# Optimization experiments

Measured on AMD Instinct MI355X. Metric: run time of the kernel, lower is better.

Reference implementation:

```python
import jax, jax.numpy as jnp
import numpy as np

HIDDEN = 1024
FFN = 2048
NUM_EXPERTS = 8
TOP_K = 2
BATCH, SEQ = 2, 1024


def setup_inputs() -> dict:
    key = jax.random.key(0)
    k0, k1, k2, k3, k4 = jax.random.split(key, 5)
    scale = 0.02
    hidden_states = jax.random.normal(k0, (BATCH, SEQ, HIDDEN), dtype=jnp.float32)
    gate_w = jax.random.normal(k1, (NUM_EXPERTS, HIDDEN), dtype=jnp.float32) * scale
    w1 = jax.random.normal(k2, (NUM_EXPERTS, FFN, HIDDEN), dtype=jnp.float32) * scale  # gate proj
    w3 = jax.random.normal(k3, (NUM_EXPERTS, FFN, HIDDEN), dtype=jnp.float32) * scale  # up proj
    w2 = jax.random.normal(k4, (NUM_EXPERTS, HIDDEN, FFN), dtype=jnp.float32) * scale  # down proj
    return {"hidden_states": hidden_states, "gate_w": gate_w, "w1": w1, "w2": w2, "w3": w3}


def reference(hidden_states, gate_w, w1, w2, w3):
    B, S, D = hidden_states.shape
    x = hidden_states.reshape(-1, D)                         # [T, D]
    T = x.shape[0]
    # Router: logits -> fp32 softmax -> top-k -> renormalize
    router_logits = jnp.einsum("td,ed->te", x, gate_w)       # [T, E]
    routing_weights = jax.nn.softmax(router_logits.astype(jnp.float32), axis=1)
    top_vals, top_idx = jax.lax.top_k(routing_weights, TOP_K)  # [T, K]
    top_vals = top_vals / jnp.sum(top_vals, axis=-1, keepdims=True)
    top_vals = top_vals.astype(x.dtype)
    # Per-token-per-expert combine weight (0 for unselected experts)
    w_te = jnp.zeros((T, NUM_EXPERTS), dtype=x.dtype)
    w_te = w_te.at[jnp.arange(T)[:, None], top_idx].add(top_vals)  # [T, E]
    # Fused experts: silu(x W1^T) * (x W3^T) -> W2^T, weighted combine
    g = jax.nn.silu(jnp.einsum("td,efd->tef", x, w1))        # [T, E, F]
    u = jnp.einsum("td,efd->tef", x, w3)                     # [T, E, F]
    y = jnp.einsum("tef,edf->ted", g * u, w2)                # [T, E, D]
    out = jnp.einsum("ted,te->td", y, w_te)                  # [T, D]
    return out.reshape(B, S, D), router_logits
```

## Files before the change

kernel.cpp:

```cpp
#include <hip/hip_runtime.h>
#include <hip/hip_bf16.h>
#include <stdint.h>

#define HIDDEN  1024
#define FFN_DIM 2048
#define NEXP    8
#define NTOK    2048
#define MAXROWS 5120

typedef short bf16x8 __attribute__((ext_vector_type(8)));
typedef float f32x4  __attribute__((ext_vector_type(4)));

static const size_t OFF_CNT  = 0;
static const size_t OFF_BASE = 64;
static const size_t OFF_TOK  = 128;
static const size_t OFF_WGT  = OFF_TOK + (size_t)NEXP*NTOK*4;
static const size_t OFF_XBF  = 131328;
static const size_t XBF_B    = (size_t)NTOK*HIDDEN*2;
static const size_t OFF_H    = OFF_XBF + XBF_B;
static const size_t H_B      = (size_t)MAXROWS*FFN_DIM*2;
static const size_t WS_NEED  = OFF_H + H_B;

__device__ __forceinline__ unsigned short f2bf(float f) {
  union { float f; unsigned u; } a; a.f = f;
  unsigned r = a.u + 0x7fff + ((a.u >> 16) & 1);
  return (unsigned short)(r >> 16);
}

__device__ __forceinline__ uint4 cvt8(float4 a, float4 b) {
  uint4 r;
  asm("v_cvt_pk_bf16_f32 %0, %1, %2" : "=v"(r.x) : "v"(a.x), "v"(a.y));
  asm("v_cvt_pk_bf16_f32 %0, %1, %2" : "=v"(r.y) : "v"(a.z), "v"(a.w));
  asm("v_cvt_pk_bf16_f32 %0, %1, %2" : "=v"(r.z) : "v"(b.x), "v"(b.y));
  asm("v_cvt_pk_bf16_f32 %0, %1, %2" : "=v"(r.w) : "v"(b.z), "v"(b.w));
  return r;
}

__device__ __forceinline__ void ld_g2l16(const void* gsrc, void* ldst) {
  __builtin_amdgcn_global_load_lds(
      (const __attribute__((address_space(1))) unsigned int*)gsrc,
      (__attribute__((address_space(3))) unsigned int*)ldst, 16, 0, 0);
}

__global__ __launch_bounds__(256) void router_kernel(
    const float* __restrict__ x, const float* __restrict__ gw,
    float* __restrict__ logits, int* __restrict__ cnt,
    int* __restrict__ tok, float* __restrict__ wgt)
{
  const int t   = blockIdx.x;
  const int tid = threadIdx.x;
  float4 xv = ((const float4*)(x + (size_t)t * HIDDEN))[tid];
  float p[NEXP];
#pragma unroll
  for (int e = 0; e < NEXP; ++e) {
    float4 gv = ((const float4*)(gw + (size_t)e * HIDDEN))[tid];
    p[e] = xv.x * gv.x + xv.y * gv.y + xv.z * gv.z + xv.w * gv.w;
  }
#pragma unroll
  for (int e = 0; e < NEXP; ++e) {
#pragma unroll
    for (int off = 32; off > 0; off >>= 1)
      p[e] += __shfl_down(p[e], off, 64);
  }
  __shared__ float red[4][NEXP];
  const int wv = tid >> 6, ln = tid & 63;
  if (ln == 0) {
#pragma unroll
    for (int e = 0; e < NEXP; ++e) red[wv][e] = p[e];
  }
  __syncthreads();
  if (tid == 0) {
    float l[NEXP];
#pragma unroll
    for (int e = 0; e < NEXP; ++e) {
      l[e] = red[0][e] + red[1][e] + red[2][e] + red[3][e];
      logits[(size_t)t * NEXP + e] = l[e];
    }
    int i0 = 0;
#pragma unroll
    for (int e = 1; e < NEXP; ++e) if (l[e] > l[i0]) i0 = e;
    int i1 = (i0 == 0) ? 1 : 0;
#pragma unroll
    for (int e = 0; e < NEXP; ++e) if (e != i0 && l[e] > l[i1]) i1 = e;
    float w0 = 1.f / (1.f + expf(l[i1] - l[i0]));
    float w1 = 1.f - w0;
    int s0 = atomicAdd(&cnt[i0], 1);
    tok[i0 * NTOK + s0] = t;  wgt[i0 * NTOK + s0] = w0;
    int s1 = atomicAdd(&cnt[i1], 1);
    tok[i1 * NTOK + s1] = t;  wgt[i1 * NTOK + s1] = w1;
  }
}

__global__ void prefix_kernel(const int* __restrict__ cnt, int* __restrict__ base) {
  if (threadIdx.x == 0 && blockIdx.x == 0) {
    int b = 0;
#pragma unroll
    for (int e = 0; e < NEXP; ++e) { base[e] = b; b += ((cnt[e] + 63) >> 6) << 6; }
    base[NEXP] = b;
  }
}

__global__ __launch_bounds__(256) void cvt_kernel(
    const float* __restrict__ src, unsigned short* __restrict__ dst, int n4)
{
  int i = blockIdx.x * blockDim.x + threadIdx.x;
  const int stride = gridDim.x * blockDim.x;
  for (; i < n4; i += stride) {
    float4 v = ((const float4*)src)[i];
    ushort4 o;
    o.x = f2bf(v.x); o.y = f2bf(v.y); o.z = f2bf(v.z); o.w = f2bf(v.w);
    ((ushort4*)dst)[i] = o;
  }
}

__global__ __launch_bounds__(512, 4) void gemm1_kernel(
    const unsigned short* __restrict__ xbf,
    const float* __restrict__ w1f,
    const float* __restrict__ w3f,
    const int* __restrict__ cnt, const int* __restrict__ base,
    const int* __restrict__ tok,
    unsigned short* __restrict__ H)
{
  const int bid  = blockIdx.x;
  const int e    = bid & 7;
  const int slot = bid >> 3;
  const int mt   = slot & 31;
  const int nt   = slot >> 5;
  const int n = cnt[e];
  if (mt * 64 >= n) return;
  const int t = threadIdx.x;
  const int w = t >> 6, l = t & 63;

  __shared__ unsigned short Xs [64 * 64];
  __shared__ unsigned short W1s[128 * 64];
  __shared__ unsigned short W3s[128 * 64];

  const int rX = t >> 3;
  const size_t tok0 = (size_t)tok[e * NTOK + min(mt * 64 + rX, n - 1)];
  const int kp = (((t & 7) ^ ((t >> 3) & 7)) << 3);

  const float* w1e = w1f + (size_t)e * FFN_DIM * HIDDEN + (size_t)(nt * 128) * HIDDEN;
  const float* w3e = w3f + (size_t)e * FFN_DIM * HIDDEN + (size_t)(nt * 128) * HIDDEN;
  const float* w1p0 = w1e + (size_t)rX        * HIDDEN + kp;
  const float* w1p1 = w1e + (size_t)(64 + rX) * HIDDEN + kp;
  const float* w3p0 = w3e + (size_t)rX        * HIDDEN + kp;
  const float* w3p1 = w3e + (size_t)(64 + rX) * HIDDEN + kp;

  uint4* lw1a = (uint4*)((char*)W1s + t * 16);
  uint4* lw1b = (uint4*)((char*)W1s + 8192 + t * 16);
  uint4* lw3a = (uint4*)((char*)W3s + t * 16);
  uint4* lw3b = (uint4*)((char*)W3s + 8192 + t * 16);
  char* ldsX = (char*)Xs + w * 1024;

  f32x4 acc1[2][2], acc3[2][2];
#pragma unroll
  for (int i = 0; i < 2; ++i)
#pragma unroll
    for (int j = 0; j < 2; ++j) { acc1[i][j] = (f32x4)0.f; acc3[i][j] = (f32x4)0.f; }

  const int Moff = (w & 1) * 32;
  const int Noff = (w >> 1) * 32;
  const int lr = l & 15;
  const int lg = l >> 4;

  for (int kb = 0; kb < HIDDEN / 64; ++kb) {
    __syncthreads();
    ld_g2l16(xbf + tok0 * HIDDEN + kb * 64 + kp, ldsX);
    {
      const int ko = kb * 64;
      float4 a0 = *(const float4*)(w1p0 + ko);
      float4 a1 = *(const float4*)(w1p0 + ko + 4);
      float4 a2 = *(const float4*)(w1p1 + ko);
      float4 a3 = *(const float4*)(w1p1 + ko + 4);
      float4 b0 = *(const float4*)(w3p0 + ko);
      float4 b1 = *(const float4*)(w3p0 + ko + 4);
      float4 b2 = *(const float4*)(w3p1 + ko);
      float4 b3 = *(const float4*)(w3p1 + ko + 4);
      *lw1a = cvt8(a0, a1);
      *lw1b = cvt8(a2, a3);
      *lw3a = cvt8(b0, b1);
      *lw3b = cvt8(b2, b3);
    }
    __syncthreads();
#pragma unroll
    for (int s = 0; s < 2; ++s) {
      const int ug = 4 * s + lg;
      bf16x8 a[2], b1v[2], b3v[2];
#pragma unroll
      for (int mi = 0; mi < 2; ++mi) {
        const int R = Moff + mi * 16 + lr;
        a[mi] = *(const bf16x8*)&Xs[R * 64 + ((ug ^ (lr & 7)) << 3)];
      }
#pragma unroll
      for (int ni = 0; ni < 2; ++ni) {
        const int R = Noff + ni * 16 + lr;
        b1v[ni] = *(const bf16x8*)&W1s[R * 64 + ((ug ^ (lr & 7)) << 3)];
        b3v[ni] = *(const bf16x8*)&W3s[R * 64 + ((ug ^ (lr & 7)) << 3)];
      }
#pragma unroll
      for (int mi = 0; mi < 2; ++mi)
#pragma unroll
        for (int ni = 0; ni < 2; ++ni) {
          acc1[mi][ni] = __builtin_amdgcn_mfma_f32_16x16x32_bf16(a[mi], b1v[ni], acc1[mi][ni], 0, 0, 0);
          acc3[mi][ni] = __builtin_amdgcn_mfma_f32_16x16x32_bf16(a[mi], b3v[ni], acc3[mi][ni], 0, 0, 0);
        }
    }
  }

  const size_t rbase = (size_t)base[e] + (size_t)mt * 64;
#pragma unroll
  for (int mi = 0; mi < 2; ++mi)
#pragma unroll
    for (int ni = 0; ni < 2; ++ni)
#pragma unroll
      for (int j = 0; j < 4; ++j) {
        int row = Moff + mi * 16 + lg * 4 + j;
        int col = nt * 128 + Noff + ni * 16 + lr;
        float s1 = acc1[mi][ni][j], s3 = acc3[mi][ni][j];
        float h = (s1 / (1.f + __expf(-s1))) * s3;
        H[(rbase + row) * FFN_DIM + col] = f2bf(h);
      }
}

__global__ __launch_bounds__(512, 4) void gemm2_kernel(
    const unsigned short* __restrict__ H,
    const float* __restrict__ w2f,
    const int* __restrict__ cnt, const int* __restrict__ base,
    const int* __restrict__ tok, const float* __restrict__ wgt,
    float* __restrict__ out)
{
  const int bid  = blockIdx.x;
  const int e    = bid & 7;
  const int slot = bid >> 3;
  const int mt   = slot & 31;
  const int nt   = (slot >> 5) & 7;
  const int sk   = slot >> 8;
  const int n = cnt[e];
  if (mt * 64 >= n) return;
  const int t = threadIdx.x;
  const int w = t >> 6, l = t & 63;

  __shared__ unsigned short Hs[64 * 64];
  __shared__ unsigned short Ws[128 * 64];
  __shared__ int   stok[64];
  __shared__ float swgt[64];

  if (t < 64) {
    int idx = mt * 64 + t;
    int ok = idx < n;
    stok[t] = ok ? tok[e * NTOK + idx] : -1;
    swgt[t] = ok ? wgt[e * NTOK + idx] : 0.f;
  }

  const int rH = t >> 3;
  const int kp = (((t & 7) ^ ((t >> 3) & 7)) << 3);
  const unsigned short* He = H + (size_t)(base[e] + mt * 64) * FFN_DIM;
  const float* w2e  = w2f + (size_t)e * HIDDEN * FFN_DIM + (size_t)(nt * 128) * FFN_DIM;
  const float* w2p0 = w2e + (size_t)rH        * FFN_DIM + kp;
  const float* w2p1 = w2e + (size_t)(64 + rH) * FFN_DIM + kp;

  uint4* lwa = (uint4*)((char*)Ws + t * 16);
  uint4* lwb = (uint4*)((char*)Ws + 8192 + t * 16);
  char* ldsH = (char*)Hs + w * 1024;

  f32x4 acc[2][2];
#pragma unroll
  for (int i = 0; i < 2; ++i)
#pragma unroll
    for (int j = 0; j < 2; ++j) acc[i][j] = (f32x4)0.f;

  const int Moff = (w & 1) * 32;
  const int Noff = (w >> 1) * 32;
  const int lr = l & 15;
  const int lg = l >> 4;
  const int kbase = sk * (FFN_DIM / 2);

  for (int kb = 0; kb < FFN_DIM / 2 / 64; ++kb) {
    __syncthreads();
    const int ko = kbase + kb * 64;
    ld_g2l16(He + (size_t)rH * FFN_DIM + ko + kp, ldsH);
    {
      float4 a0 = *(const float4*)(w2p0 + ko);
      float4 a1 = *(const float4*)(w2p0 + ko + 4);
      float4 a2 = *(const float4*)(w2p1 + ko);
      float4 a3 = *(const float4*)(w2p1 + ko + 4);
      *lwa = cvt8(a0, a1);
      *lwb = cvt8(a2, a3);
    }
    __syncthreads();
#pragma unroll
    for (int s = 0; s < 2; ++s) {
      const int ug = 4 * s + lg;
      bf16x8 a[2], b[2];
#pragma unroll
      for (int mi = 0; mi < 2; ++mi) {
        const int R = Moff + mi * 16 + lr;
        a[mi] = *(const bf16x8*)&Hs[R * 64 + ((ug ^ (lr & 7)) << 3)];
      }
#pragma unroll
      for (int ni = 0; ni < 2; ++ni) {
        const int R = Noff + ni * 16 + lr;
        b[ni] = *(const bf16x8*)&Ws[R * 64 + ((ug ^ (lr & 7)) << 3)];
      }
#pragma unroll
      for (int mi = 0; mi < 2; ++mi)
#pragma unroll
        for (int ni = 0; ni < 2; ++ni)
          acc[mi][ni] = __builtin_amdgcn_mfma_f32_16x16x32_bf16(a[mi], b[ni], acc[mi][ni], 0, 0, 0);
    }
  }

#pragma unroll
  for (int mi = 0; mi < 2; ++mi)
#pragma unroll
    for (int ni = 0; ni < 2; ++ni)
#pragma unroll
      for (int j = 0; j < 4; ++j) {
        int row = Moff + mi * 16 + lg * 4 + j;
        int tk = stok[row];
        if (tk >= 0) {
          int col = nt * 128 + Noff + ni * 16 + lr;
          atomicAdd(&out[(size_t)tk * HIDDEN + col], swgt[row] * acc[mi][ni][j]);
        }
      }
}

#define TT 12
#define FC 256
#define NCHUNK (FFN_DIM / FC)

__global__ __launch_bounds__(256) void moe_ffn_kernel(
    const float* __restrict__ x,
    const float* __restrict__ w1, const float* __restrict__ w2,
    const float* __restrict__ w3,
    const int* __restrict__ cnt, const int* __restrict__ tok,
    const float* __restrict__ wgt, float* __restrict__ out)
{
  const int e  = blockIdx.y;
  const int n  = cnt[e];
  const int ts = blockIdx.x * TT;
  if (ts >= n) return;
  const int tid = threadIdx.x;

  __shared__ float xs[TT * HIDDEN];
  __shared__ float hc[TT * FC];
  __shared__ int   stok[TT];
  __shared__ float swgt[TT];

  if (tid < TT) {
    int idx = ts + tid;
    int tk  = (idx < n) ? tok[e * NTOK + idx] : -1;
    stok[tid] = tk;
    swgt[tid] = (idx < n) ? wgt[e * NTOK + idx] : 0.f;
  }
  __syncthreads();
#pragma unroll
  for (int i = 0; i < TT; ++i) {
    int tk = stok[i];
    float4 v = make_float4(0.f, 0.f, 0.f, 0.f);
    if (tk >= 0) v = ((const float4*)(x + (size_t)tk * HIDDEN))[tid];
    ((float4*)(xs + i * HIDDEN))[tid] = v;
  }
  __syncthreads();

  const float* w1e = w1 + (size_t)e * FFN_DIM * HIDDEN;
  const float* w3e = w3 + (size_t)e * FFN_DIM * HIDDEN;
  const float* w2e = w2 + (size_t)e * HIDDEN * FFN_DIM;

  float yacc[4][TT];
#pragma unroll
  for (int j = 0; j < 4; ++j)
#pragma unroll
    for (int t = 0; t < TT; ++t) yacc[j][t] = 0.f;

  for (int c = 0; c < NCHUNK; ++c) {
    const int f = c * FC + tid;
    const float4* r1 = (const float4*)(w1e + (size_t)f * HIDDEN);
    const float4* r3 = (const float4*)(w3e + (size_t)f * HIDDEN);
    float a1[TT], a3[TT];
#pragma unroll
    for (int t = 0; t < TT; ++t) { a1[t] = 0.f; a3[t] = 0.f; }
    for (int k = 0; k < HIDDEN / 4; ++k) {
      float4 v1 = r1[k];
      float4 v3 = r3[k];
#pragma unroll
      for (int t = 0; t < TT; ++t) {
        float4 xv = *(const float4*)(xs + t * HIDDEN + 4 * k);
        a1[t] += xv.x * v1.x + xv.y * v1.y + xv.z * v1.z + xv.w * v1.w;
        a3[t] += xv.x * v3.x + xv.y * v3.y + xv.z * v3.z + xv.w * v3.w;
      }
    }
    __syncthreads();
#pragma unroll
    for (int t = 0; t < TT; ++t) {
      float g  = a1[t];
      float sg = g / (1.f + __expf(-g));
      hc[t * FC + tid] = sg * a3[t];
    }
    __syncthreads();
    const float4* r20 = (const float4*)(w2e + (size_t)(tid      ) * FFN_DIM + c * FC);
    const float4* r21 = (const float4*)(w2e + (size_t)(tid + 256) * FFN_DIM + c * FC);
    const float4* r22 = (const float4*)(w2e + (size_t)(tid + 512) * FFN_DIM + c * FC);
    const float4* r23 = (const float4*)(w2e + (size_t)(tid + 768) * FFN_DIM + c * FC);
    for (int k = 0; k < FC / 4; ++k) {
      float4 wv0 = r20[k], wv1 = r21[k], wv2 = r22[k], wv3 = r23[k];
#pragma unroll
      for (int t = 0; t < TT; ++t) {
        float4 hv = *(const float4*)(hc + t * FC + 4 * k);
        yacc[0][t] += hv.x * wv0.x + hv.y * wv0.y + hv.z * wv0.z + hv.w * wv0.w;
        yacc[1][t] += hv.x * wv1.x + hv.y * wv1.y + hv.z * wv1.z + hv.w * wv1.w;
        yacc[2][t] += hv.x * wv2.x + hv.y * wv2.y + hv.z * wv2.z + hv.w * wv2.w;
        yacc[3][t] += hv.x * wv3.x + hv.y * wv3.y + hv.z * wv3.z + hv.w * wv3.w;
      }
    }
  }

#pragma unroll
  for (int t = 0; t < TT; ++t) {
    int tk = stok[t];
    if (tk < 0) continue;
    float wt = swgt[t];
    float* orow = out + (size_t)tk * HIDDEN;
    atomicAdd(orow + tid,       wt * yacc[0][t]);
    atomicAdd(orow + tid + 256, wt * yacc[1][t]);
    atomicAdd(orow + tid + 512, wt * yacc[2][t]);
    atomicAdd(orow + tid + 768, wt * yacc[3][t]);
  }
}

extern "C" void kernel_launch(void* const* d_in, const int* in_sizes, int n_in,
                              void* d_out, int out_size, void* d_ws, size_t ws_size,
                              hipStream_t stream) {
  const float* x  = (const float*)d_in[0];
  const float* gw = (const float*)d_in[1];
  const float* w1 = (const float*)d_in[2];
  const float* w2 = (const float*)d_in[3];
  const float* w3 = (const float*)d_in[4];
  float* out    = (float*)d_out;
  float* logits = out + (size_t)NTOK * HIDDEN;

  char* ws = (char*)d_ws;
  int*   cnt  = (int*)(ws + OFF_CNT);
  int*   base = (int*)(ws + OFF_BASE);
  int*   tokp = (int*)(ws + OFF_TOK);
  float* wgtp = (float*)(ws + OFF_WGT);

  hipMemsetAsync(out, 0, (size_t)NTOK * HIDDEN * sizeof(float), stream);
  hipMemsetAsync(cnt, 0, NEXP * sizeof(int), stream);

  router_kernel<<<NTOK, 256, 0, stream>>>(x, gw, logits, cnt, tokp, wgtp);

  if (ws_size >= WS_NEED) {
    unsigned short* xbf  = (unsigned short*)(ws + OFF_XBF);
    unsigned short* Hbuf = (unsigned short*)(ws + OFF_H);

    cvt_kernel<<<512, 256, 0, stream>>>(x, xbf, (int)(NTOK * HIDDEN / 4));
    prefix_kernel<<<1, 64, 0, stream>>>(cnt, base);

    gemm1_kernel<<<NEXP * 32 * 16, 512, 0, stream>>>(xbf, w1, w3, cnt, base, tokp, Hbuf);
    gemm2_kernel<<<NEXP * 32 * 8 * 2, 512, 0, stream>>>(Hbuf, w2, cnt, base, tokp, wgtp, out);
  } else {
    dim3 grid((NTOK + TT - 1) / TT, NEXP);
    moe_ffn_kernel<<<grid, 256, 0, stream>>>(x, w1, w2, w3, cnt, tokp, wgtp, out);
  }
}
```

Baseline: 217.5 us.

## Double-buffer LDS in expert GEMMs, retile gemm1 to 128x64, fuse x cast into router

Both expert GEMMs now use double-buffered shared-memory tiles: the next k-slice is fetched from global memory while the current slice feeds the MFMAs, leaving one barrier per iteration instead of two. gemm1 changes its tile from 64 tokens x 128 FFN columns to 128 tokens x 64 columns. This halves the fp32 weight traffic per block, which now reads the w1/w3 fp32 weights once per 128 tokens, and expert padding moves to 128 rows. The separate fp32-to-bf16 cast kernel is folded into the router, which already loads each token row, removing one launch and one pass over x. The cost is more LDS per block and more padded rows for small experts, which may reduce occupancy.

```diff
diff --git a/kernel.cpp b/kernel.cpp
--- a/kernel.cpp
+++ b/kernel.cpp
@@ -45,11 +45,17 @@
 __global__ __launch_bounds__(256) void router_kernel(
     const float* __restrict__ x, const float* __restrict__ gw,
     float* __restrict__ logits, int* __restrict__ cnt,
-    int* __restrict__ tok, float* __restrict__ wgt)
+    int* __restrict__ tok, float* __restrict__ wgt,
+    unsigned short* __restrict__ xbf)
 {
   const int t   = blockIdx.x;
   const int tid = threadIdx.x;
   float4 xv = ((const float4*)(x + (size_t)t * HIDDEN))[tid];
+  if (xbf) {
+    ushort4 o;
+    o.x = f2bf(xv.x); o.y = f2bf(xv.y); o.z = f2bf(xv.z); o.w = f2bf(xv.w);
+    ((ushort4*)(xbf + (size_t)t * HIDDEN))[tid] = o;
+  }
   float p[NEXP];
 #pragma unroll
   for (int e = 0; e < NEXP; ++e) {
@@ -95,23 +101,35 @@
   if (threadIdx.x == 0 && blockIdx.x == 0) {
     int b = 0;
 #pragma unroll
-    for (int e = 0; e < NEXP; ++e) { base[e] = b; b += ((cnt[e] + 63) >> 6) << 6; }
+    for (int e = 0; e < NEXP; ++e) { base[e] = b; b += ((cnt[e] + 127) >> 7) << 7; }
     base[NEXP] = b;
   }
 }
 
-__global__ __launch_bounds__(256) void cvt_kernel(
-    const float* __restrict__ src, unsigned short* __restrict__ dst, int n4)
-{
-  int i = blockIdx.x * blockDim.x + threadIdx.x;
-  const int stride = gridDim.x * blockDim.x;
-  for (; i < n4; i += stride) {
-    float4 v = ((const float4*)src)[i];
-    ushort4 o;
-    o.x = f2bf(v.x); o.y = f2bf(v.y); o.z = f2bf(v.z); o.w = f2bf(v.w);
-    ((ushort4*)dst)[i] = o;
-  }
-}
+#define G1_COMPUTE(BUF)                                                                           \
+  {                                                                                               \
+    const unsigned short* Xc  = Xs[BUF];                                                          \
+    const unsigned short* W1c = W1s[BUF];                                                         \
+    const unsigned short* W3c = W3s[BUF];                                                         \
+    _Pragma("unroll")                                                                             \
+    for (int s = 0; s < 2; ++s) {                                                                 \
+      const int sw = (((4 * s + lg) ^ (lr & 7)) << 3);                                            \
+      bf16x8 a0v = *(const bf16x8*)&Xc[(Moff + lr) * 64 + sw];                                    \
+      bf16x8 a1v = *(const bf16x8*)&Xc[(Moff + 16 + lr) * 64 + sw];                               \
+      bf16x8 p0  = *(const bf16x8*)&W1c[(Noff + lr) * 64 + sw];                                   \
+      bf16x8 p1  = *(const bf16x8*)&W1c[(Noff + 16 + lr) * 64 + sw];                              \
+      bf16x8 q0  = *(const bf16x8*)&W3c[(Noff + lr) * 64 + sw];                                   \
+      bf16x8 q1  = *(const bf16x8*)&W3c[(Noff + 16 + lr) * 64 + sw];                              \
+      acc1[0][0] = __builtin_amdgcn_mfma_f32_16x16x32_bf16(a0v, p0, acc1[0][0], 0, 0, 0);         \
+      acc1[0][1] = __builtin_amdgcn_mfma_f32_16x16x32_bf16(a0v, p1, acc1[0][1], 0, 0, 0);         \
+      acc1[1][0] = __builtin_amdgcn_mfma_f32_16x16x32_bf16(a1v, p0, acc1[1][0], 0, 0, 0);         \
+      acc1[1][1] = __builtin_amdgcn_mfma_f32_16x16x32_bf16(a1v, p1, acc1[1][1], 0, 0, 0);         \
+      acc3[0][0] = __builtin_amdgcn_mfma_f32_16x16x32_bf16(a0v, q0, acc3[0][0], 0, 0, 0);         \
+      acc3[0][1] = __builtin_amdgcn_mfma_f32_16x16x32_bf16(a0v, q1, acc3[0][1], 0, 0, 0);         \
+      acc3[1][0] = __builtin_amdgcn_mfma_f32_16x16x32_bf16(a1v, q0, acc3[1][0], 0, 0, 0);         \
+      acc3[1][1] = __builtin_amdgcn_mfma_f32_16x16x32_bf16(a1v, q1, acc3[1][1], 0, 0, 0);         \
+    }                                                                                             \
+  }
 
 __global__ __launch_bounds__(512, 4) void gemm1_kernel(
     const unsigned short* __restrict__ xbf,
@@ -124,33 +142,24 @@
   const int bid  = blockIdx.x;
   const int e    = bid & 7;
   const int slot = bid >> 3;
-  const int mt   = slot & 31;
-  const int nt   = slot >> 5;
+  const int mt   = slot & 15;
+  const int nt   = slot >> 4;
   const int n = cnt[e];
-  if (mt * 64 >= n) return;
+  if (mt * 128 >= n) return;
   const int t = threadIdx.x;
   const int w = t >> 6, l = t & 63;
 
-  __shared__ unsigned short Xs [64 * 64];
-  __shared__ unsigned short W1s[128 * 64];
-  __shared__ unsigned short W3s[128 * 64];
+  __shared__ unsigned short Xs [2][128 * 64];
+  __shared__ unsigned short W1s[2][64 * 64];
+  __shared__ unsigned short W3s[2][64 * 64];
 
   const int rX = t >> 3;
-  const size_t tok0 = (size_t)tok[e * NTOK + min(mt * 64 + rX, n - 1)];
+  const size_t tok0 = (size_t)tok[e * NTOK + min(mt * 128 + rX, n - 1)];
+  const size_t tok1 = (size_t)tok[e * NTOK + min(mt * 128 + 64 + rX, n - 1)];
   const int kp = (((t & 7) ^ ((t >> 3) & 7)) << 3);
 
-  const float* w1e = w1f + (size_t)e * FFN_DIM * HIDDEN + (size_t)(nt * 128) * HIDDEN;
-  const float* w3e = w3f + (size_t)e * FFN_DIM * HIDDEN + (size_t)(nt * 128) * HIDDEN;
-  const float* w1p0 = w1e + (size_t)rX        * HIDDEN + kp;
-  const float* w1p1 = w1e + (size_t)(64 + rX) * HIDDEN + kp;
-  const float* w3p0 = w3e + (size_t)rX        * HIDDEN + kp;
-  const float* w3p1 = w3e + (size_t)(64 + rX) * HIDDEN + kp;
-
-  uint4* lw1a = (uint4*)((char*)W1s + t * 16);
-  uint4* lw1b = (uint4*)((char*)W1s + 8192 + t * 16);
-  uint4* lw3a = (uint4*)((char*)W3s + t * 16);
-  uint4* lw3b = (uint4*)((char*)W3s + 8192 + t * 16);
-  char* ldsX = (char*)Xs + w * 1024;
+  const float* w1p = w1f + (size_t)e * FFN_DIM * HIDDEN + ((size_t)nt * 64 + rX) * HIDDEN + kp;
+  const float* w3p = w3f + (size_t)e * FFN_DIM * HIDDEN + ((size_t)nt * 64 + rX) * HIDDEN + kp;
 
   f32x4 acc1[2][2], acc3[2][2];
 #pragma unroll
@@ -158,56 +167,41 @@
 #pragma unroll
     for (int j = 0; j < 2; ++j) { acc1[i][j] = (f32x4)0.f; acc3[i][j] = (f32x4)0.f; }
 
-  const int Moff = (w & 1) * 32;
-  const int Noff = (w >> 1) * 32;
+  const int Moff = (w & 3) * 32;
+  const int Noff = (w >> 2) * 32;
   const int lr = l & 15;
   const int lg = l >> 4;
 
-  for (int kb = 0; kb < HIDDEN / 64; ++kb) {
+  ld_g2l16(xbf + tok0 * HIDDEN + kp, (char*)Xs[0] + w * 1024);
+  ld_g2l16(xbf + tok1 * HIDDEN + kp, (char*)Xs[0] + 8192 + w * 1024);
+  {
+    float4 a0 = *(const float4*)(w1p);
+    float4 a1 = *(const float4*)(w1p + 4);
+    float4 b0 = *(const float4*)(w3p);
+    float4 b1 = *(const float4*)(w3p + 4);
+    *(uint4*)((char*)W1s[0] + t * 16) = cvt8(a0, a1);
+    *(uint4*)((char*)W3s[0] + t * 16) = cvt8(b0, b1);
+  }
+  __syncthreads();
+
+  int cur = 0;
+  for (int kb = 0; kb < HIDDEN / 64 - 1; ++kb) {
+    const int ko = (kb + 1) * 64;
+    ld_g2l16(xbf + tok0 * HIDDEN + ko + kp, (char*)Xs[cur ^ 1] + w * 1024);
+    ld_g2l16(xbf + tok1 * HIDDEN + ko + kp, (char*)Xs[cur ^ 1] + 8192 + w * 1024);
+    float4 a0 = *(const float4*)(w1p + ko);
+    float4 a1 = *(const float4*)(w1p + ko + 4);
+    float4 b0 = *(const float4*)(w3p + ko);
+    float4 b1 = *(const float4*)(w3p + ko + 4);
+    G1_COMPUTE(cur);
+    *(uint4*)((char*)W1s[cur ^ 1] + t * 16) = cvt8(a0, a1);
+    *(uint4*)((char*)W3s[cur ^ 1] + t * 16) = cvt8(b0, b1);
     __syncthreads();
-    ld_g2l16(xbf + tok0 * HIDDEN + kb * 64 + kp, ldsX);
-    {
-      const int ko = kb * 64;
-      float4 a0 = *(const float4*)(w1p0 + ko);
-      float4 a1 = *(const float4*)(w1p0 + ko + 4);
-      float4 a2 = *(const float4*)(w1p1 + ko);
-      float4 a3 = *(const float4*)(w1p1 + ko + 4);
-      float4 b0 = *(const float4*)(w3p0 + ko);
-      float4 b1 = *(const float4*)(w3p0 + ko + 4);
-      float4 b2 = *(const float4*)(w3p1 + ko);
-      float4 b3 = *(const float4*)(w3p1 + ko + 4);
-      *lw1a = cvt8(a0, a1);
-      *lw1b = cvt8(a2, a3);
-      *lw3a = cvt8(b0, b1);
-      *lw3b = cvt8(b2, b3);
-    }
-    __syncthreads();
-#pragma unroll
-    for (int s = 0; s < 2; ++s) {
-      const int ug = 4 * s + lg;
-      bf16x8 a[2], b1v[2], b3v[2];
-#pragma unroll
-      for (int mi = 0; mi < 2; ++mi) {
-        const int R = Moff + mi * 16 + lr;
-        a[mi] = *(const bf16x8*)&Xs[R * 64 + ((ug ^ (lr & 7)) << 3)];
-      }
-#pragma unroll
-      for (int ni = 0; ni < 2; ++ni) {
-        const int R = Noff + ni * 16 + lr;
-        b1v[ni] = *(const bf16x8*)&W1s[R * 64 + ((ug ^ (lr & 7)) << 3)];
-        b3v[ni] = *(const bf16x8*)&W3s[R * 64 + ((ug ^ (lr & 7)) << 3)];
-      }
-#pragma unroll
-      for (int mi = 0; mi < 2; ++mi)
-#pragma unroll
-        for (int ni = 0; ni < 2; ++ni) {
-          acc1[mi][ni] = __builtin_amdgcn_mfma_f32_16x16x32_bf16(a[mi], b1v[ni], acc1[mi][ni], 0, 0, 0);
-          acc3[mi][ni] = __builtin_amdgcn_mfma_f32_16x16x32_bf16(a[mi], b3v[ni], acc3[mi][ni], 0, 0, 0);
-        }
-    }
-  }
-
-  const size_t rbase = (size_t)base[e] + (size_t)mt * 64;
+    cur ^= 1;
+  }
+  G1_COMPUTE(cur);
+
+  const size_t rbase = (size_t)base[e] + (size_t)mt * 128;
 #pragma unroll
   for (int mi = 0; mi < 2; ++mi)
 #pragma unroll
@@ -215,12 +209,30 @@
 #pragma unroll
       for (int j = 0; j < 4; ++j) {
         int row = Moff + mi * 16 + lg * 4 + j;
-        int col = nt * 128 + Noff + ni * 16 + lr;
+        int col = nt * 64 + Noff + ni * 16 + lr;
         float s1 = acc1[mi][ni][j], s3 = acc3[mi][ni][j];
         float h = (s1 / (1.f + __expf(-s1))) * s3;
         H[(rbase + row) * FFN_DIM + col] = f2bf(h);
       }
 }
+
+#define G2_COMPUTE(BUF)                                                                           \
+  {                                                                                               \
+    const unsigned short* Hc = Hs[BUF];                                                           \
+    const unsigned short* Wc = Ws[BUF];                                                           \
+    _Pragma("unroll")                                                                             \
+    for (int s = 0; s < 2; ++s) {                                                                 \
+      const int sw = (((4 * s + lg) ^ (lr & 7)) << 3);                                            \
+      bf16x8 a0v = *(const bf16x8*)&Hc[(Moff + lr) * 64 + sw];                                    \
+      bf16x8 a1v = *(const bf16x8*)&Hc[(Moff + 16 + lr) * 64 + sw];                               \
+      bf16x8 p0  = *(const bf16x8*)&Wc[(Noff + lr) * 64 + sw];                                    \
+      bf16x8 p1  = *(const bf16x8*)&Wc[(Noff + 16 + lr) * 64 + sw];                               \
+      acc[0][0] = __builtin_amdgcn_mfma_f32_16x16x32_bf16(a0v, p0, acc[0][0], 0, 0, 0);           \
+      acc[0][1] = __builtin_amdgcn_mfma_f32_16x16x32_bf16(a0v, p1, acc[0][1], 0, 0, 0);           \
+      acc[1][0] = __builtin_amdgcn_mfma_f32_16x16x32_bf16(a1v, p0, acc[1][0], 0, 0, 0);           \
+      acc[1][1] = __builtin_amdgcn_mfma_f32_16x16x32_bf16(a1v, p1, acc[1][1], 0, 0, 0);           \
+    }                                                                                             \
+  }
 
 __global__ __launch_bounds__(512, 4) void gemm2_kernel(
     const unsigned short* __restrict__ H,
@@ -240,8 +252,8 @@
   const int t = threadIdx.x;
   const int w = t >> 6, l = t & 63;
 
-  __shared__ unsigned short Hs[64 * 64];
-  __shared__ unsigned short Ws[128 * 64];
+  __shared__ unsigned short Hs[2][64 * 64];
+  __shared__ unsigned short Ws[2][128 * 64];
   __shared__ int   stok[64];
   __shared__ float swgt[64];
 
@@ -254,14 +266,10 @@
 
   const int rH = t >> 3;
   const int kp = (((t & 7) ^ ((t >> 3) & 7)) << 3);
-  const unsigned short* He = H + (size_t)(base[e] + mt * 64) * FFN_DIM;
-  const float* w2e  = w2f + (size_t)e * HIDDEN * FFN_DIM + (size_t)(nt * 128) * FFN_DIM;
-  const float* w2p0 = w2e + (size_t)rH        * FFN_DIM + kp;
-  const float* w2p1 = w2e + (size_t)(64 + rH) * FFN_DIM + kp;
-
-  uint4* lwa = (uint4*)((char*)Ws + t * 16);
-  uint4* lwb = (uint4*)((char*)Ws + 8192 + t * 16);
-  char* ldsH = (char*)Hs + w * 1024;
+  const unsigned short* Hp = H + (size_t)(base[e] + mt * 64 + rH) * FFN_DIM + sk * (FFN_DIM / 2) + kp;
+  const float* w2b  = w2f + (size_t)e * HIDDEN * FFN_DIM + sk * (FFN_DIM / 2) + kp;
+  const float* w2p0 = w2b + ((size_t)nt * 128 + rH) * FFN_DIM;
+  const float* w2p1 = w2b + ((size_t)nt * 128 + 64 + rH) * FFN_DIM;
 
   f32x4 acc[2][2];
 #pragma unroll
@@ -273,42 +281,33 @@
   const int Noff = (w >> 1) * 32;
   const int lr = l & 15;
   const int lg = l >> 4;
-  const int kbase = sk * (FFN_DIM / 2);
-
-  for (int kb = 0; kb < FFN_DIM / 2 / 64; ++kb) {
+
+  ld_g2l16(Hp, (char*)Hs[0] + w * 1024);
+  {
+    float4 a0 = *(const float4*)(w2p0);
+    float4 a1 = *(const float4*)(w2p0 + 4);
+    float4 a2 = *(const float4*)(w2p1);
+    float4 a3 = *(const float4*)(w2p1 + 4);
+    *(uint4*)((char*)Ws[0] + t * 16)        = cvt8(a0, a1);
+    *(uint4*)((char*)Ws[0] + 8192 + t * 16) = cvt8(a2, a3);
+  }
+  __syncthreads();
+
+  int cur = 0;
+  for (int kb = 0; kb < FFN_DIM / 2 / 64 - 1; ++kb) {
+    const int ko = (kb + 1) * 64;
+    ld_g2l16(Hp + ko, (char*)Hs[cur ^ 1] + w * 1024);
+    float4 a0 = *(const float4*)(w2p0 + ko);
+    float4 a1 = *(const float4*)(w2p0 + ko + 4);
+    float4 a2 = *(const float4*)(w2p1 + ko);
+    float4 a3 = *(const float4*)(w2p1 + ko + 4);
+    G2_COMPUTE(cur);
+    *(uint4*)((char*)Ws[cur ^ 1] + t * 16)        = cvt8(a0, a1);
+    *(uint4*)((char*)Ws[cur ^ 1] + 8192 + t * 16) = cvt8(a2, a3);
     __syncthreads();
-    const int ko = kbase + kb * 64;
-    ld_g2l16(He + (size_t)rH * FFN_DIM + ko + kp, ldsH);
-    {
-      float4 a0 = *(const float4*)(w2p0 + ko);
-      float4 a1 = *(const float4*)(w2p0 + ko + 4);
-      float4 a2 = *(const float4*)(w2p1 + ko);
-      float4 a3 = *(const float4*)(w2p1 + ko + 4);
-      *lwa = cvt8(a0, a1);
-      *lwb = cvt8(a2, a3);
-    }
-    __syncthreads();
-#pragma unroll
-    for (int s = 0; s < 2; ++s) {
-      const int ug = 4 * s + lg;
-      bf16x8 a[2], b[2];
-#pragma unroll
-      for (int mi = 0; mi < 2; ++mi) {
-        const int R = Moff + mi * 16 + lr;
-        a[mi] = *(const bf16x8*)&Hs[R * 64 + ((ug ^ (lr & 7)) << 3)];
-      }
-#pragma unroll
-      for (int ni = 0; ni < 2; ++ni) {
-        const int R = Noff + ni * 16 + lr;
-        b[ni] = *(const bf16x8*)&Ws[R * 64 + ((ug ^ (lr & 7)) << 3)];
-      }
-#pragma unroll
-      for (int mi = 0; mi < 2; ++mi)
-#pragma unroll
-        for (int ni = 0; ni < 2; ++ni)
-          acc[mi][ni] = __builtin_amdgcn_mfma_f32_16x16x32_bf16(a[mi], b[ni], acc[mi][ni], 0, 0, 0);
-    }
-  }
+    cur ^= 1;
+  }
+  G2_COMPUTE(cur);
 
 #pragma unroll
   for (int mi = 0; mi < 2; ++mi)
@@ -445,19 +444,18 @@
   int*   tokp = (int*)(ws + OFF_TOK);
   float* wgtp = (float*)(ws + OFF_WGT);
 
+  const bool big = (ws_size >= WS_NEED);
+  unsigned short* xbf  = big ? (unsigned short*)(ws + OFF_XBF) : (unsigned short*)0;
+  unsigned short* Hbuf = big ? (unsigned short*)(ws + OFF_H)   : (unsigned short*)0;
+
   hipMemsetAsync(out, 0, (size_t)NTOK * HIDDEN * sizeof(float), stream);
   hipMemsetAsync(cnt, 0, NEXP * sizeof(int), stream);
 
-  router_kernel<<<NTOK, 256, 0, stream>>>(x, gw, logits, cnt, tokp, wgtp);
-
-  if (ws_size >= WS_NEED) {
-    unsigned short* xbf  = (unsigned short*)(ws + OFF_XBF);
-    unsigned short* Hbuf = (unsigned short*)(ws + OFF_H);
-
-    cvt_kernel<<<512, 256, 0, stream>>>(x, xbf, (int)(NTOK * HIDDEN / 4));
+  router_kernel<<<NTOK, 256, 0, stream>>>(x, gw, logits, cnt, tokp, wgtp, xbf);
+
+  if (big) {
     prefix_kernel<<<1, 64, 0, stream>>>(cnt, base);
-
-    gemm1_kernel<<<NEXP * 32 * 16, 512, 0, stream>>>(xbf, w1, w3, cnt, base, tokp, Hbuf);
+    gemm1_kernel<<<NEXP * 16 * 32, 512, 0, stream>>>(xbf, w1, w3, cnt, base, tokp, Hbuf);
     gemm2_kernel<<<NEXP * 32 * 8 * 2, 512, 0, stream>>>(Hbuf, w2, cnt, base, tokp, wgtp, out);
   } else {
     dim3 grid((NTOK + TT - 1) / TT, NEXP);
```

Result: faster. 209.0 us (-3.9%).
